# Kernel tuning notes

Hardware: AMD Instinct MI355X
Metric: run time of the kernel (lower is better)

The kernel has to match this reference:

```python
import jax, jax.numpy as jnp
import numpy as np

N = 100000
E = 6400000
NT_DIM = 8
HID = 32


def setup_inputs() -> dict:
    key = jax.random.key(0)
    k1, k2, k3, k4, k5, k6, k7 = jax.random.split(key, 7)
    nt_emb = jax.random.normal(k1, (N, NT_DIM), dtype=jnp.float32)
    edge_index = jax.random.randint(k2, (2, E), 0, N, dtype=jnp.int64)
    lm_mask = jax.random.uniform(k3, (N,), dtype=jnp.float32)
    fan_in1 = 2 * NT_DIM + 2
    lim1 = 1.0 / np.sqrt(fan_in1)
    W1 = jax.random.uniform(k4, (fan_in1, HID), minval=-lim1, maxval=lim1, dtype=jnp.float32)
    b1 = jax.random.uniform(k5, (HID,), minval=-lim1, maxval=lim1, dtype=jnp.float32)
    lim2 = 1.0 / np.sqrt(HID)
    W2 = jax.random.uniform(k6, (HID, 1), minval=-lim2, maxval=lim2, dtype=jnp.float32)
    b2 = jax.random.uniform(k7, (1,), minval=-lim2, maxval=lim2, dtype=jnp.float32)
    return {"nt_emb": nt_emb, "edge_index": edge_index, "lm_mask": lm_mask,
            "W1": W1, "b1": b1, "W2": W2, "b2": b2}


def reference(nt_emb, edge_index, lm_mask, W1, b1, W2, b2):
    s, d = edge_index[0], edge_index[1]
    # [E, 2*nt_dim + 2] edge features: src emb, dst emb, src mask, dst mask
    feat = jnp.concatenate(
        [nt_emb[s], nt_emb[d], lm_mask[s][:, None], lm_mask[d][:, None]], axis=-1)
    h = jax.nn.relu(feat @ W1 + b1)          # [E, hid]
    out = jax.nn.sigmoid(h @ W2 + b2)        # [E, 1]
    return out[:, 0]                         # [E]
```

## Files before the change

### kernel.cpp

```cpp
#include <hip/hip_runtime.h>
#include <hip/hip_bf16.h>

typedef short short8 __attribute__((ext_vector_type(8)));
typedef float floatx4 __attribute__((ext_vector_type(4)));

#define HID 32
#define NTD 8
#define FAN_IN 18

__device__ __forceinline__ short f2bf(float f) {
    union { float f; unsigned u; } v; v.f = f;
    unsigned r = v.u + 0x7fffu + ((v.u >> 16) & 1u);
    return (short)(r >> 16);
}

__global__ void build_table(const float* __restrict__ emb,
                            const float* __restrict__ mask,
                            short* __restrict__ T, int N) {
    int n = blockIdx.x * blockDim.x + threadIdx.x;
    if (n >= N) return;
    const float4* p = (const float4*)(emb + (size_t)n * NTD);
    float4 lo = p[0], hi = p[1];
    short8 a, b;
    a[0] = f2bf(lo.x); a[1] = f2bf(lo.y); a[2] = f2bf(lo.z); a[3] = f2bf(lo.w);
    a[4] = f2bf(hi.x); a[5] = f2bf(hi.y); a[6] = f2bf(hi.z); a[7] = f2bf(hi.w);
    b[0] = f2bf(mask[n]); b[1] = (short)0x3F80;
    b[2] = b[3] = b[4] = b[5] = b[6] = b[7] = 0;
    short8* row = (short8*)(T + (size_t)n * 16);
    row[0] = a; row[1] = b;
}

template <int ESZ>
__device__ __forceinline__ void load_idx(const char* __restrict__ sideBase,
                                         long long base, long long E, int r,
                                         int idx[4]) {
    long long e0 = base + 4 * r;
    if (base + 64 <= E) {
        if (ESZ == 8) {
            const int4* ip = (const int4*)(sideBase + e0 * 8);
            int4 w0 = ip[0], w1 = ip[1];
            idx[0] = w0.x; idx[1] = w0.z; idx[2] = w1.x; idx[3] = w1.z;
        } else {
            int4 w0 = *(const int4*)(sideBase + e0 * 4);
            idx[0] = w0.x; idx[1] = w0.y; idx[2] = w0.z; idx[3] = w0.w;
        }
    } else {
        #pragma unroll
        for (int t = 0; t < 4; ++t) {
            long long e = e0 + t;
            if (e >= E) e = E - 1;
            idx[t] = *(const int*)(sideBase + e * ESZ);
        }
    }
}

template <int ESZ>
__device__ void run_loop(const char* __restrict__ ei,
                         const short* __restrict__ T,
                         float* __restrict__ out, long long E,
                         short8 a0, short8 a1,
                         const float* w2v0, const float* w2v1, float bias2,
                         long long waveId, long long nWaves, int g, int r) {
    const long long nGroups = (E + 63) >> 6;
    const char* sideBase = ei + (g >= 2 ? (size_t)E * ESZ : 0);
    const int halfOff = (g & 1) * 16;

    long long grp = waveId;
    int idx[4] = {0, 0, 0, 0};
    if (grp < nGroups) load_idx<ESZ>(sideBase, grp << 6, E, r, idx);

    while (grp < nGroups) {
        const long long base = grp << 6;
        const long long nxt = grp + nWaves;

        short8 fb0 = *(const short8*)((const char*)T + (size_t)(unsigned)idx[0] * 32 + halfOff);
        short8 fb1 = *(const short8*)((const char*)T + (size_t)(unsigned)idx[1] * 32 + halfOff);
        short8 fb2 = *(const short8*)((const char*)T + (size_t)(unsigned)idx[2] * 32 + halfOff);
        short8 fb3 = *(const short8*)((const char*)T + (size_t)(unsigned)idx[3] * 32 + halfOff);

        int idxn[4] = {0, 0, 0, 0};
        if (nxt < nGroups) load_idx<ESZ>(sideBase, nxt << 6, E, r, idxn);

        float vals[4];
        #pragma unroll
        for (int t = 0; t < 4; ++t) {
            short8 fb = (t == 0) ? fb0 : (t == 1) ? fb1 : (t == 2) ? fb2 : fb3;
            floatx4 acc0 = {0.f, 0.f, 0.f, 0.f};
            floatx4 acc1 = {0.f, 0.f, 0.f, 0.f};
            acc0 = __builtin_amdgcn_mfma_f32_16x16x32_bf16(a0, fb, acc0, 0, 0, 0);
            acc1 = __builtin_amdgcn_mfma_f32_16x16x32_bf16(a1, fb, acc1, 0, 0, 0);
            float partial = 0.f;
            #pragma unroll
            for (int q = 0; q < 4; ++q) {
                partial += fmaxf(acc0[q], 0.f) * w2v0[q];
                partial += fmaxf(acc1[q], 0.f) * w2v1[q];
            }
            partial += __shfl_xor(partial, 16, 64);
            partial += __shfl_xor(partial, 32, 64);
            vals[t] = 1.0f / (1.0f + __expf(-(partial + bias2)));
        }

        if (g == 0) {
            long long e0 = base + 4 * r;
            if (base + 64 <= E) {
                float4 v4 = {vals[0], vals[1], vals[2], vals[3]};
                *(float4*)(out + e0) = v4;
            } else {
                #pragma unroll
                for (int t = 0; t < 4; ++t)
                    if (e0 + t < E) out[e0 + t] = vals[t];
            }
        }

        idx[0] = idxn[0]; idx[1] = idxn[1]; idx[2] = idxn[2]; idx[3] = idxn[3];
        grp = nxt;
    }
}

__global__ __launch_bounds__(256, 4) void lg_table_kernel(
    const char* __restrict__ ei_bytes,
    const short* __restrict__ T,
    const float* __restrict__ W1,
    const float* __restrict__ b1,
    const float* __restrict__ W2,
    const float* __restrict__ b2,
    float* __restrict__ out,
    long long E)
{
    const int lane = threadIdx.x & 63;
    const int waveInBlock = threadIdx.x >> 6;
    const long long waveId = (long long)blockIdx.x * (blockDim.x >> 6) + waveInBlock;
    const long long nWaves = (long long)gridDim.x * (blockDim.x >> 6);

    const int* ei32 = (const int*)ei_bytes;
    int probe = ei32[2 * lane + 1];
    unsigned long long nz = __ballot(probe != 0);
    const int esz = (nz == 0ull) ? 8 : 4;

    const int r = lane & 15;
    const int g = lane >> 4;

    short8 a0, a1;
    #pragma unroll
    for (int j = 0; j < 8; ++j) {
        int k = g * 8 + j;
        float v0 = 0.f, v1 = 0.f;
        if (k < 8)                    { v0 = W1[k * HID + r];        v1 = W1[k * HID + 16 + r]; }
        else if (k == 8)              { v0 = W1[16 * HID + r];       v1 = W1[16 * HID + 16 + r]; }
        else if (k == 9)              { v0 = b1[r];                  v1 = b1[16 + r]; }
        else if (k >= 16 && k < 24)   { v0 = W1[(k - 8) * HID + r];  v1 = W1[(k - 8) * HID + 16 + r]; }
        else if (k == 24)             { v0 = W1[17 * HID + r];       v1 = W1[17 * HID + 16 + r]; }
        a0[j] = f2bf(v0);
        a1[j] = f2bf(v1);
    }

    float w2v0[4], w2v1[4];
    #pragma unroll
    for (int q = 0; q < 4; ++q) {
        w2v0[q] = W2[g * 4 + q];
        w2v1[q] = W2[16 + g * 4 + q];
    }
    const float bias2 = b2[0];

    if (esz == 8)
        run_loop<8>(ei_bytes, T, out, E, a0, a1, w2v0, w2v1, bias2, waveId, nWaves, g, r);
    else
        run_loop<4>(ei_bytes, T, out, E, a0, a1, w2v0, w2v1, bias2, waveId, nWaves, g, r);
}

__global__ __launch_bounds__(256, 4) void lg_kernel(
    const float* __restrict__ nt_emb,
    const char* __restrict__ ei_bytes,
    const float* __restrict__ lm_mask,
    const float* __restrict__ W1,
    const float* __restrict__ b1,
    const float* __restrict__ W2,
    const float* __restrict__ b2,
    float* __restrict__ out,
    long long E)
{
    const int lane = threadIdx.x & 63;
    const int waveInBlock = threadIdx.x >> 6;
    const long long waveId = (long long)blockIdx.x * (blockDim.x >> 6) + waveInBlock;
    const long long nWaves = (long long)gridDim.x * (blockDim.x >> 6);

    const int* ei32 = (const int*)ei_bytes;
    int probe = ei32[2 * lane + 1];
    unsigned long long nz = __ballot(probe != 0);
    const long long esz = (nz == 0ull) ? 8 : 4;

    const int r = lane & 15;
    const int g = lane >> 4;

    short8 a0, a1;
    #pragma unroll
    for (int j = 0; j < 8; ++j) {
        int k = g * 8 + j;
        float v0 = 0.f, v1 = 0.f;
        if (k < FAN_IN)       { v0 = W1[k * HID + r];      v1 = W1[k * HID + 16 + r]; }
        else if (k == FAN_IN) { v0 = b1[r];                v1 = b1[16 + r]; }
        a0[j] = f2bf(v0);
        a1[j] = f2bf(v1);
    }

    float w2v0[4], w2v1[4];
    #pragma unroll
    for (int q = 0; q < 4; ++q) {
        w2v0[q] = W2[g * 4 + q];
        w2v1[q] = W2[16 + g * 4 + q];
    }
    const float bias2 = b2[0];

    const long long nGroups = (E + 15) >> 4;
    for (long long grp = waveId; grp < nGroups; grp += nWaves) {
        long long e = (grp << 4) + r;
        const bool valid = (e < E);
        long long ec = valid ? e : (E - 1);

        int s = *(const int*)(ei_bytes + ec * esz);
        int d = *(const int*)(ei_bytes + (E + ec) * esz);

        short8 fb;
        #pragma unroll
        for (int j = 0; j < 8; ++j) fb[j] = 0;
        if (g < 2) {
            const float4* p = (const float4*)(nt_emb + (long long)(g == 0 ? s : d) * NTD);
            float4 lo = p[0];
            float4 hi = p[1];
            fb[0] = f2bf(lo.x); fb[1] = f2bf(lo.y); fb[2] = f2bf(lo.z); fb[3] = f2bf(lo.w);
            fb[4] = f2bf(hi.x); fb[5] = f2bf(hi.y); fb[6] = f2bf(hi.z); fb[7] = f2bf(hi.w);
        } else if (g == 2) {
            fb[0] = f2bf(lm_mask[s]);
            fb[1] = f2bf(lm_mask[d]);
            fb[2] = (short)0x3F80;
        }

        floatx4 acc0 = {0.f, 0.f, 0.f, 0.f};
        floatx4 acc1 = {0.f, 0.f, 0.f, 0.f};
        acc0 = __builtin_amdgcn_mfma_f32_16x16x32_bf16(a0, fb, acc0, 0, 0, 0);
        acc1 = __builtin_amdgcn_mfma_f32_16x16x32_bf16(a1, fb, acc1, 0, 0, 0);

        float partial = 0.f;
        #pragma unroll
        for (int q = 0; q < 4; ++q) {
            partial += fmaxf(acc0[q], 0.f) * w2v0[q];
            partial += fmaxf(acc1[q], 0.f) * w2v1[q];
        }
        partial += __shfl_xor(partial, 16, 64);
        partial += __shfl_xor(partial, 32, 64);

        float val = 1.0f / (1.0f + __expf(-(partial + bias2)));
        if (g == 0 && valid) out[e] = val;
    }
}

extern "C" void kernel_launch(void* const* d_in, const int* in_sizes, int n_in,
                              void* d_out, int out_size, void* d_ws, size_t ws_size,
                              hipStream_t stream) {
    const float* nt_emb = (const float*)d_in[0];
    const char*  ei     = (const char*)d_in[1];
    const float* lm     = (const float*)d_in[2];
    const float* W1     = (const float*)d_in[3];
    const float* b1     = (const float*)d_in[4];
    const float* W2     = (const float*)d_in[5];
    const float* b2     = (const float*)d_in[6];
    float* out = (float*)d_out;

    long long E = (long long)in_sizes[1] / 2;
    int N = in_sizes[2];

    size_t tableBytes = (size_t)N * 32;
    if (ws_size >= tableBytes) {
        short* T = (short*)d_ws;
        build_table<<<dim3((N + 255) / 256), dim3(256), 0, stream>>>(nt_emb, lm, T, N);
        lg_table_kernel<<<dim3(2048), dim3(256), 0, stream>>>(ei, T, W1, b1, W2, b2, out, E);
    } else {
        lg_kernel<<<dim3(2048), dim3(256), 0, stream>>>(nt_emb, ei, lm, W1, b1, W2, b2, out, E);
    }
}
```

Baseline: 82.62 us.

## Deepen gather prefetch and compute second layer with MFMA

Restructures the edge loop into a deeper software pipeline: the table rows for the next group are gathered while the current group computes, and indices are loaded two groups ahead. The second layer (dot with W2) now runs as a third bf16 MFMA over packed ReLU outputs instead of per-lane FMAs plus cross-lane shuffles. The sigmoid uses hardware exp2 and rcp. The goal is to hide gather latency and cut VALU and shuffle work. The cost is more registers and bf16 rounding of the hidden activations.

```diff
diff --git a/kernel.cpp b/kernel.cpp
--- a/kernel.cpp
+++ b/kernel.cpp
@@ -12,6 +12,17 @@
     union { float f; unsigned u; } v; v.f = f;
     unsigned r = v.u + 0x7fffu + ((v.u >> 16) & 1u);
     return (short)(r >> 16);
+}
+
+__device__ __forceinline__ unsigned cvt_pk_bf16(float lo, float hi) {
+    unsigned r;
+    asm("v_cvt_pk_bf16_f32 %0, %1, %2" : "=v"(r) : "v"(lo), "v"(hi));
+    return r;
+}
+
+__device__ __forceinline__ float fast_sigmoid(float x) {
+    float e = __builtin_amdgcn_exp2f(x * -1.44269504f);
+    return __builtin_amdgcn_rcpf(1.0f + e);
 }
 
 __global__ void build_table(const float* __restrict__ emb,
@@ -31,89 +42,106 @@
 }
 
 template <int ESZ>
-__device__ __forceinline__ void load_idx(const char* __restrict__ sideBase,
-                                         long long base, long long E, int r,
-                                         int idx[4]) {
-    long long e0 = base + 4 * r;
+__device__ __forceinline__ int4 load_idx4(const char* __restrict__ sideBase,
+                                          long long grp, long long nGroups,
+                                          long long E, int r) {
+    long long g = (grp < nGroups) ? grp : (nGroups - 1);
+    long long base = g << 6;
+    long long e0 = base + 4 * (long long)r;
+    int4 v;
     if (base + 64 <= E) {
         if (ESZ == 8) {
-            const int4* ip = (const int4*)(sideBase + e0 * 8);
+            const int4* ip = (const int4*)(sideBase + (size_t)e0 * 8);
             int4 w0 = ip[0], w1 = ip[1];
-            idx[0] = w0.x; idx[1] = w0.z; idx[2] = w1.x; idx[3] = w1.z;
+            v.x = w0.x; v.y = w0.z; v.z = w1.x; v.w = w1.z;
         } else {
-            int4 w0 = *(const int4*)(sideBase + e0 * 4);
-            idx[0] = w0.x; idx[1] = w0.y; idx[2] = w0.z; idx[3] = w0.w;
+            v = *(const int4*)(sideBase + (size_t)e0 * 4);
         }
     } else {
-        #pragma unroll
-        for (int t = 0; t < 4; ++t) {
-            long long e = e0 + t;
-            if (e >= E) e = E - 1;
-            idx[t] = *(const int*)(sideBase + e * ESZ);
-        }
-    }
+        long long em = E - 1;
+        long long ea = e0     < em ? e0     : em;
+        long long eb = e0 + 1 < em ? e0 + 1 : em;
+        long long ec = e0 + 2 < em ? e0 + 2 : em;
+        long long ed = e0 + 3 < em ? e0 + 3 : em;
+        v.x = *(const int*)(sideBase + (size_t)ea * ESZ);
+        v.y = *(const int*)(sideBase + (size_t)eb * ESZ);
+        v.z = *(const int*)(sideBase + (size_t)ec * ESZ);
+        v.w = *(const int*)(sideBase + (size_t)ed * ESZ);
+    }
+    return v;
+}
+
+__device__ __forceinline__ short8 gath(const char* __restrict__ Tc, int idx, unsigned halfOff) {
+    return *(const short8*)(Tc + ((unsigned)idx * 32u + halfOff));
+}
+
+__device__ __forceinline__ float edge_logit(short8 a0, short8 a1, short8 a2, short8 fb) {
+    floatx4 z = {0.f, 0.f, 0.f, 0.f};
+    floatx4 h0 = __builtin_amdgcn_mfma_f32_16x16x32_bf16(a0, fb, z, 0, 0, 0);
+    floatx4 h1 = __builtin_amdgcn_mfma_f32_16x16x32_bf16(a1, fb, z, 0, 0, 0);
+    unsigned u0 = cvt_pk_bf16(fmaxf(h0[0], 0.f), fmaxf(h0[1], 0.f));
+    unsigned u1 = cvt_pk_bf16(fmaxf(h0[2], 0.f), fmaxf(h0[3], 0.f));
+    unsigned u2 = cvt_pk_bf16(fmaxf(h1[0], 0.f), fmaxf(h1[1], 0.f));
+    unsigned u3 = cvt_pk_bf16(fmaxf(h1[2], 0.f), fmaxf(h1[3], 0.f));
+    int4 bu; bu.x = (int)u0; bu.y = (int)u1; bu.z = (int)u2; bu.w = (int)u3;
+    short8 b2 = __builtin_bit_cast(short8, bu);
+    floatx4 o = __builtin_amdgcn_mfma_f32_16x16x32_bf16(a2, b2, z, 0, 0, 0);
+    return o[0];
 }
 
 template <int ESZ>
 __device__ void run_loop(const char* __restrict__ ei,
-                         const short* __restrict__ T,
+                         const char* __restrict__ Tc,
                          float* __restrict__ out, long long E,
-                         short8 a0, short8 a1,
-                         const float* w2v0, const float* w2v1, float bias2,
+                         short8 a0, short8 a1, short8 a2, float bias2,
                          long long waveId, long long nWaves, int g, int r) {
     const long long nGroups = (E + 63) >> 6;
     const char* sideBase = ei + (g >= 2 ? (size_t)E * ESZ : 0);
-    const int halfOff = (g & 1) * 16;
-
-    long long grp = waveId;
-    int idx[4] = {0, 0, 0, 0};
-    if (grp < nGroups) load_idx<ESZ>(sideBase, grp << 6, E, r, idx);
-
-    while (grp < nGroups) {
-        const long long base = grp << 6;
-        const long long nxt = grp + nWaves;
-
-        short8 fb0 = *(const short8*)((const char*)T + (size_t)(unsigned)idx[0] * 32 + halfOff);
-        short8 fb1 = *(const short8*)((const char*)T + (size_t)(unsigned)idx[1] * 32 + halfOff);
-        short8 fb2 = *(const short8*)((const char*)T + (size_t)(unsigned)idx[2] * 32 + halfOff);
-        short8 fb3 = *(const short8*)((const char*)T + (size_t)(unsigned)idx[3] * 32 + halfOff);
-
-        int idxn[4] = {0, 0, 0, 0};
-        if (nxt < nGroups) load_idx<ESZ>(sideBase, nxt << 6, E, r, idxn);
-
-        float vals[4];
-        #pragma unroll
-        for (int t = 0; t < 4; ++t) {
-            short8 fb = (t == 0) ? fb0 : (t == 1) ? fb1 : (t == 2) ? fb2 : fb3;
-            floatx4 acc0 = {0.f, 0.f, 0.f, 0.f};
-            floatx4 acc1 = {0.f, 0.f, 0.f, 0.f};
-            acc0 = __builtin_amdgcn_mfma_f32_16x16x32_bf16(a0, fb, acc0, 0, 0, 0);
-            acc1 = __builtin_amdgcn_mfma_f32_16x16x32_bf16(a1, fb, acc1, 0, 0, 0);
-            float partial = 0.f;
-            #pragma unroll
-            for (int q = 0; q < 4; ++q) {
-                partial += fmaxf(acc0[q], 0.f) * w2v0[q];
-                partial += fmaxf(acc1[q], 0.f) * w2v1[q];
-            }
-            partial += __shfl_xor(partial, 16, 64);
-            partial += __shfl_xor(partial, 32, 64);
-            vals[t] = 1.0f / (1.0f + __expf(-(partial + bias2)));
-        }
-
+    const unsigned halfOff = (unsigned)(g & 1) * 16u;
+
+    if (waveId >= nGroups) return;
+
+    long long cur = waveId;
+    long long nxt = cur + nWaves;
+
+    int4 ic = load_idx4<ESZ>(sideBase, cur, nGroups, E, r);
+    short8 fc0 = gath(Tc, ic.x, halfOff);
+    short8 fc1 = gath(Tc, ic.y, halfOff);
+    short8 fc2 = gath(Tc, ic.z, halfOff);
+    short8 fc3 = gath(Tc, ic.w, halfOff);
+    int4 in0 = load_idx4<ESZ>(sideBase, nxt, nGroups, E, r);
+
+    while (true) {
+        short8 fn0 = gath(Tc, in0.x, halfOff);
+        short8 fn1 = gath(Tc, in0.y, halfOff);
+        short8 fn2 = gath(Tc, in0.z, halfOff);
+        short8 fn3 = gath(Tc, in0.w, halfOff);
+        int4 in1 = load_idx4<ESZ>(sideBase, nxt + nWaves, nGroups, E, r);
+
+        float v0 = fast_sigmoid(edge_logit(a0, a1, a2, fc0) + bias2);
+        float v1 = fast_sigmoid(edge_logit(a0, a1, a2, fc1) + bias2);
+        float v2 = fast_sigmoid(edge_logit(a0, a1, a2, fc2) + bias2);
+        float v3 = fast_sigmoid(edge_logit(a0, a1, a2, fc3) + bias2);
+
+        long long base = cur << 6;
         if (g == 0) {
-            long long e0 = base + 4 * r;
+            long long e0 = base + 4 * (long long)r;
             if (base + 64 <= E) {
-                float4 v4 = {vals[0], vals[1], vals[2], vals[3]};
-                *(float4*)(out + e0) = v4;
+                float4 st; st.x = v0; st.y = v1; st.z = v2; st.w = v3;
+                *(float4*)(out + e0) = st;
             } else {
-                #pragma unroll
-                for (int t = 0; t < 4; ++t)
-                    if (e0 + t < E) out[e0 + t] = vals[t];
+                if (e0     < E) out[e0]     = v0;
+                if (e0 + 1 < E) out[e0 + 1] = v1;
+                if (e0 + 2 < E) out[e0 + 2] = v2;
+                if (e0 + 3 < E) out[e0 + 3] = v3;
             }
         }
 
-        idx[0] = idxn[0]; idx[1] = idxn[1]; idx[2] = idxn[2]; idx[3] = idxn[3];
-        grp = nxt;
+        cur = nxt;
+        if (cur >= nGroups) break;
+        nxt = cur + nWaves;
+        fc0 = fn0; fc1 = fn1; fc2 = fn2; fc3 = fn3;
+        in0 = in1;
     }
 }
 
@@ -154,18 +182,19 @@
         a1[j] = f2bf(v1);
     }
 
-    float w2v0[4], w2v1[4];
+    short8 a2;
     #pragma unroll
-    for (int q = 0; q < 4; ++q) {
-        w2v0[q] = W2[g * 4 + q];
-        w2v1[q] = W2[16 + g * 4 + q];
-    }
+    for (int j = 0; j < 8; ++j) {
+        int p = (j < 4) ? (g * 4 + j) : (16 + g * 4 + (j - 4));
+        a2[j] = (r == 0) ? f2bf(W2[p]) : (short)0;
+    }
+
     const float bias2 = b2[0];
 
     if (esz == 8)
-        run_loop<8>(ei_bytes, T, out, E, a0, a1, w2v0, w2v1, bias2, waveId, nWaves, g, r);
+        run_loop<8>(ei_bytes, (const char*)T, out, E, a0, a1, a2, bias2, waveId, nWaves, g, r);
     else
-        run_loop<4>(ei_bytes, T, out, E, a0, a1, w2v0, w2v1, bias2, waveId, nWaves, g, r);
+        run_loop<4>(ei_bytes, (const char*)T, out, E, a0, a1, a2, bias2, waveId, nWaves, g, r);
 }
 
 __global__ __launch_bounds__(256, 4) void lg_kernel(
@@ -249,7 +278,7 @@
         partial += __shfl_xor(partial, 16, 64);
         partial += __shfl_xor(partial, 32, 64);
 
-        float val = 1.0f / (1.0f + __expf(-(partial + bias2)));
+        float val = fast_sigmoid(partial + bias2);
         if (g == 0 && valid) out[e] = val;
     }
 }
```

After: 90.70 us. 9.8% more time.
